# Kernel optimization log

Measured on AMD Instinct MI355X. Metric: run time of the kernel, lower is better.

## Reference

```python
import jax, jax.numpy as jnp
import numpy as np

B, N, S, T_STEPS = 8, 150, 22, 1000
E = 2 * N - 1  # 299
M = 32


def quat_mul(a, b):
    # Hamilton product, quats as (w, x, y, z)
    aw, ax, ay, az = a[..., 0], a[..., 1], a[..., 2], a[..., 3]
    bw, bx, by, bz = b[..., 0], b[..., 1], b[..., 2], b[..., 3]
    return jnp.stack([
        aw * bw - ax * bx - ay * by - az * bz,
        aw * bx + ax * bw + ay * bz - az * by,
        aw * by - ax * bz + ay * bw + az * bx,
        aw * bz + ax * by - ay * bx + az * bw,
    ], axis=-1)


def quat_conj(q):
    return q * jnp.array([1.0, -1.0, -1.0, -1.0], q.dtype)


def quat_rotate(q, v):
    # rotate vector v by unit quaternion q
    w, qv = q[..., :1], q[..., 1:]
    t = 2.0 * jnp.cross(qv, v)
    return v + w * t + jnp.cross(qv, t)


def egnn_layer(q, x, h, e, mask_f, Wm, bm, Wf, bf, Wq, bq):
    Bb, Nn = h.shape[0], h.shape[-2]
    eye = jnp.eye(Nn, dtype=h.dtype)
    mm = mask_f[:, :, None] * mask_f[:, None, :] * (1.0 - eye)  # [B,N,N]
    n_nodes = mask_f.sum(-1)  # [B]
    q_i = q[:, :, None, :]
    q_j = q[:, None, :, :]
    x_i = x[:, :, None, :]
    x_j = x[:, None, :, :]
    qj_inv = quat_conj(q_j)
    diff = x_i - x_j                              # [B,N,N,3]
    local_x = quat_rotate(qj_inv, diff)           # R_j^T (x_i - x_j)
    local_q = quat_mul(quat_mul(qj_inv, q_i), q_j)  # q_j^-1 q_i q_j
    d2 = jnp.sum(diff * diff, -1)                 # [B,N,N]
    dot = jnp.abs(jnp.sum(q_i * q_j, -1))         # [B,N,N]
    hi = jnp.broadcast_to(h[:, :, None, :], (Bb, Nn, Nn, h.shape[-1]))
    hj = jnp.broadcast_to(h[:, None, :, :], (Bb, Nn, Nn, h.shape[-1]))
    feat = jnp.concatenate([hi, hj, e, local_x, local_q, d2[..., None], dot[..., None]], -1)
    m = (feat @ Wm + bm) * mm[..., None]          # [B,N,N,M]
    o = jnp.concatenate([h, m.sum(-2)], -1) @ Wf + bf
    delta = (m @ Wq + bq) * mm[..., None]         # [B,N,N,6]
    upd_x = (quat_rotate(q_j, local_x + delta[..., 3:]) + x_j).sum(-2) \
        / (n_nodes[:, None, None] - 1.0)
    vec_q = jnp.concatenate([jnp.zeros_like(delta[..., :1]), delta[..., :3]], -1)
    s = (local_q + quat_mul(local_q, vec_q)).sum(-2)  # [B,N,4]
    local_upd_q = s / jnp.maximum(jnp.linalg.norm(s, axis=-1, keepdims=True), 1e-12)
    upd_q = quat_mul(quat_mul(q, local_upd_q), quat_conj(q))
    return upd_q, upd_x, o


def relposenc():
    r = jnp.arange(N)
    rel = N - 1 + (r[:, None] - r[None, :])
    return jax.nn.one_hot(rel, E, dtype=jnp.float32)  # [N,N,E]


def setup_inputs() -> dict:
    key = jax.random.key(0)
    ks = jax.random.split(key, 32)
    quats = jax.random.normal(ks[0], (B, N, 4), dtype=jnp.float32)
    quats = quats / jnp.linalg.norm(quats, axis=-1, keepdims=True)
    trans = jax.random.normal(ks[1], (B, N, 3), dtype=jnp.float32) * 10.0
    features = jax.random.uniform(ks[2], (B, N, S), dtype=jnp.float32)
    mask = jnp.ones((B, N), dtype=bool)
    inp = {"quats": quats, "trans": trans, "features": features, "mask": mask, "t": 250}
    # (message_in, feature_in, feature_out) per layer; H1=30, I=64
    dims = [(2 * 30 + E + 9, 30 + M, 64), (2 * 64 + E + 9, 64 + M, 64),
            (2 * 64 + E + 9, 64 + M, 64), (2 * 64 + E + 9, 64 + M, 1)]
    k = 3
    for i, (mi, fi, fo) in enumerate(dims, 1):
        inp[f"wm{i}"] = jax.random.normal(ks[k], (mi, M), dtype=jnp.float32) / np.float32(np.sqrt(mi)); k += 1
        inp[f"bm{i}"] = jnp.zeros((M,), jnp.float32)
        inp[f"wf{i}"] = jax.random.normal(ks[k], (fi, fo), dtype=jnp.float32) / np.float32(np.sqrt(fi)); k += 1
        inp[f"bf{i}"] = jnp.zeros((fo,), jnp.float32)
        inp[f"wq{i}"] = jax.random.normal(ks[k], (M, 6), dtype=jnp.float32) / np.float32(np.sqrt(M)); k += 1
        inp[f"bq{i}"] = jnp.zeros((6,), jnp.float32)
    return inp


def reference(quats, trans, features,
              wm1, bm1, wf1, bf1, wq1, bq1,
              wm2, bm2, wf2, bf2, wq2, bq2,
              wm3, bm3, wf3, bf3, wq3, bq3,
              wm4, bm4, wf4, bf4, wq4, bq4,
              mask, t):
    mask_f = mask.astype(quats.dtype)
    ft = jnp.full((B, N, 1), t / T_STEPS, dtype=quats.dtype)
    h = jnp.concatenate([quats, trans, features, ft], -1)  # [B,N,30]
    e = jnp.broadcast_to(relposenc()[None], (B, N, N, E))
    q, x = quats, trans
    q, x, i1 = egnn_layer(q, x, h, e, mask_f, wm1, bm1, wf1, bf1, wq1, bq1)
    q, x, i2 = egnn_layer(q, x, jax.nn.relu(i1), e, mask_f, wm2, bm2, wf2, bf2, wq2, bq2)
    q, x, i3 = egnn_layer(q, x, jax.nn.relu(i2), e, mask_f, wm3, bm3, wf3, bf3, wq3, bq3)
    q, x, _ = egnn_layer(q, x, jax.nn.relu(i3), e, mask_f, wm4, bm4, wf4, bf4, wq4, bq4)
    return jnp.concatenate([q, x], -1)  # tensor_7 of final frames [B,N,7]
```

## Files before the change

kernel.cpp:

```cpp
#include <hip/hip_runtime.h>
#include <math.h>

#define NB 8
#define NN 150
#define NE 299
#define NNODE (NB*NN)

struct Quat { float w, x, y, z; };

__device__ inline Quat qmul(Quat a, Quat b) {
    Quat r;
    r.w = a.w*b.w - a.x*b.x - a.y*b.y - a.z*b.z;
    r.x = a.w*b.x + a.x*b.w + a.y*b.z - a.z*b.y;
    r.y = a.w*b.y - a.x*b.z + a.y*b.w + a.z*b.x;
    r.z = a.w*b.z + a.x*b.y - a.y*b.x + a.z*b.w;
    return r;
}
__device__ inline Quat qconj(Quat a) { return Quat{a.w, -a.x, -a.y, -a.z}; }

__device__ inline float3 qrot(Quat q, float3 v) {
    float tx = 2.f*(q.y*v.z - q.z*v.y);
    float ty = 2.f*(q.z*v.x - q.x*v.z);
    float tz = 2.f*(q.x*v.y - q.y*v.x);
    float cx = q.y*tz - q.z*ty;
    float cy = q.z*tx - q.x*tz;
    float cz = q.x*ty - q.y*tx;
    float3 r;
    r.x = v.x + q.w*tx + cx;
    r.y = v.y + q.w*ty + cy;
    r.z = v.z + q.w*tz + cz;
    return r;
}

struct InitArgs {
    const float* quats; const float* trans; const float* feats; const int* tptr;
    const float* wm[4]; const float* wq[4];
    const float* bm1; const float* bq1;
    float* h; float* A; float* C0; float* Ad; float* Cd0;
    float* P; float* Ed; float* Gq;
};

__global__ __launch_bounds__(256) void init_kernel(InitArgs a)
{
    __shared__ float sh[8][30];
    __shared__ float sA[8][32];
    __shared__ float sC[8][32];
    __shared__ float sPS[256];
    const int tid = threadIdx.x;
    const int blk = blockIdx.x;

    if (blk < 150) {
        const int nodeBase = blk*8;
        for (int idx = tid; idx < 8*30; idx += 256) {
            const int nl = idx / 30;
            const int d  = idx - nl*30;
            const int n  = nodeBase + nl;
            float v;
            if      (d < 4)  v = a.quats[n*4 + d];
            else if (d < 7)  v = a.trans[n*3 + (d-4)];
            else if (d < 29) v = a.feats[n*22 + (d-7)];
            else             v = (float)a.tptr[0] * (1.0f/1000.0f);
            sh[nl][d] = v;
            a.h[n*64 + d] = v;
        }
        __syncthreads();
        {
            const int nl = tid >> 5;
            const int k  = tid & 31;
            const int n  = nodeBase + nl;
            float av = a.bm1[k], cv = 0.f;
#pragma unroll
            for (int d = 0; d < 30; ++d) {
                const float hv = sh[nl][d];
                av = fmaf(hv, a.wm[0][d*32 + k], av);
                cv = fmaf(hv, a.wm[0][(30+d)*32 + k], cv);
            }
            a.A[n*32 + k]  = av;
            a.C0[n*32 + k] = cv;
            sA[nl][k] = av;
            sC[nl][k] = cv;
        }
        __syncthreads();
        if (tid < 96) {
            const int half = (tid >= 48) ? 1 : 0;
            const int idx  = tid - half*48;
            const int nl = idx / 6;
            const int d  = idx - nl*6;
            const float* src = half ? sC[nl] : sA[nl];
            float acc = half ? 0.f : a.bq1[d];
#pragma unroll
            for (int k = 0; k < 32; ++k) acc = fmaf(src[k], a.wq[0][k*6 + d], acc);
            (half ? a.Cd0 : a.Ad)[(nodeBase+nl)*8 + d] = acc;
        }
    } else if (blk < 154) {
        const int l = blk - 150;
        const int HDl = (l == 0) ? 30 : 64;
        const float* E = a.wm[l] + 2*HDl*32;
        float* Pl = a.P + l*9600;
        const int g = tid >> 5, k = tid & 31;
        const int r0 = g*38;
        float part = 0.f;
        for (int r = r0; r < r0+38 && r < NE; ++r) part += E[r*32 + k];
        sPS[g*32 + k] = part;
        __syncthreads();
        float run = 0.f;
        for (int gg = 0; gg < g; ++gg) run += sPS[gg*32 + k];
        const int rw = (r0+38 < 300) ? r0+38 : 300;
        for (int r = r0; r < rw; ++r) {
            Pl[r*32 + k] = run;
            if (r < NE) run += E[r*32 + k];
        }
    } else if (blk < 158) {
        const int l = blk - 154;
        const int HDl = (l == 0) ? 30 : 64;
        const float* E  = a.wm[l] + 2*HDl*32;
        const float* Wq = a.wq[l];
        if (tid < 54) {
            const int t = tid/6, d = tid - t*6;
            float acc = 0.f;
#pragma unroll
            for (int k = 0; k < 32; ++k) acc = fmaf(E[(NE+t)*32 + k], Wq[k*6 + d], acc);
            a.Gq[l*64 + t*6 + d] = acc;
        }
    } else {
        const int bb = blk - 158;
        const int l = bb / 25;
        const int rbase = (bb % 25) * 12;
        const int HDl = (l == 0) ? 30 : 64;
        const float* E  = a.wm[l] + 2*HDl*32;
        const float* Wq = a.wq[l];
        if (tid < 72) {
            const int rr = tid/6, d = tid - rr*6;
            const int r = rbase + rr;
            if (r < NE) {
                float acc = 0.f;
#pragma unroll
                for (int k = 0; k < 32; ++k) acc = fmaf(E[r*32 + k], Wq[k*6 + d], acc);
                a.Ed[l*2400 + r*8 + d] = acc;
            }
        }
    }
}

struct PairArgs {
    const float* qcur; const float* xcur;
    const float* hbuf; const float* Abuf;
    const float* Cin;  const float* Adin; const float* Cdin;
    const float* Ed;   const float* Gq;   const float* P;
    const float* wm;   const float* wf;   const float* bf;
    const float* wmN;  const float* bmN;
    const float* wqN;  const float* bqN;
    float* hout; float* Aout; float* Adout;
    float* Cout; float* Cdout;
    float* qout; float* xout; float* dout;
};

template<int HD, bool COMPUTE_O, bool WRITE_OUT>
__global__ __launch_bounds__(192, 4) void pair_kernel(PairArgs a)
{
    constexpr int STR  = 196;
    constexpr int NROW = COMPUTE_O ? 32 : 7;
    constexpr int NV   = COMPUTE_O ? 16 : 7;
    __shared__ __align__(16) float sMat[NROW*STR];
    __shared__ float sWmG[COMPUTE_O ? 288 : 4];
    __shared__ float sPr[192];
    __shared__ float sTot[16];
    __shared__ float sCs[32];
    __shared__ float sHi[64], sO[64], sMs[32];
    __shared__ float sGq[54], sAd[6];
    __shared__ float sA2[32], sC2[32];

    const int tid   = threadIdx.x;
    const int nodeI = blockIdx.x;
    const int b     = nodeI / NN;
    const int i     = nodeI - b*NN;

    if (COMPUTE_O) {
        for (int idx = tid; idx < 288; idx += 192) sWmG[idx] = a.wm[(2*HD+NE)*32 + idx];
        for (int idx = tid; idx < HD;  idx += 192) sHi[idx]  = a.hbuf[nodeI*64 + idx];
    }
    if (tid < 54) sGq[tid] = a.Gq[tid];
    if (tid >= 64 && tid < 70) sAd[tid-64] = a.Adin[nodeI*8 + (tid-64)];
    __syncthreads();

    const Quat  qi = {a.qcur[nodeI*4+0], a.qcur[nodeI*4+1],
                      a.qcur[nodeI*4+2], a.qcur[nodeI*4+3]};
    const float3 xi = {a.xcur[nodeI*3+0], a.xcur[nodeI*3+1], a.xcur[nodeI*3+2]};

    float vals[NV];
#pragma unroll
    for (int v = 0; v < NV; ++v) vals[v] = 0.f;

    const int j = tid;
    Quat qj = {1.f,0.f,0.f,0.f};
    const float mm = (j == i) ? 0.f : 1.f;
    if (j < NN) {
        const int nodeJ = b*NN + j;
        qj = Quat{a.qcur[nodeJ*4+0], a.qcur[nodeJ*4+1],
                  a.qcur[nodeJ*4+2], a.qcur[nodeJ*4+3]};
        float3 xj = {a.xcur[nodeJ*3+0], a.xcur[nodeJ*3+1], a.xcur[nodeJ*3+2]};
        float3 diff = {xi.x - xj.x, xi.y - xj.y, xi.z - xj.z};
        Quat qjc = qconj(qj);
        float3 lx = qrot(qjc, diff);
        Quat lq = qmul(qmul(qjc, qi), qj);
        const float d2 = diff.x*diff.x + diff.y*diff.y + diff.z*diff.z;
        const float dt = fabsf(qi.w*qj.w + qi.x*qj.x + qi.y*qj.y + qi.z*qj.z);
        const float g[9] = {lx.x, lx.y, lx.z, lq.w, lq.x, lq.y, lq.z, d2, dt};

        const float4* cd4 = (const float4*)(a.Cdin + nodeJ*8);
        const float4* ed4 = (const float4*)(a.Ed + (NN-1 + i - j)*8);
        const float4 c0 = cd4[0], c1 = cd4[1];
        const float4 e0 = ed4[0], e1 = ed4[1];
        float delta[6];
        delta[0] = sAd[0] + c0.x + e0.x;
        delta[1] = sAd[1] + c0.y + e0.y;
        delta[2] = sAd[2] + c0.z + e0.z;
        delta[3] = sAd[3] + c0.w + e0.w;
        delta[4] = sAd[4] + c1.x + e1.x;
        delta[5] = sAd[5] + c1.y + e1.y;
#pragma unroll
        for (int t = 0; t < 9; ++t) {
            const float gv = g[t];
#pragma unroll
            for (int d = 0; d < 6; ++d)
                delta[d] = fmaf(gv, sGq[t*6 + d], delta[d]);
        }
#pragma unroll
        for (int d = 0; d < 6; ++d) delta[d] *= mm;

        constexpr int vo = COMPUTE_O ? 9 : 0;
        if (COMPUTE_O) {
#pragma unroll
            for (int t = 0; t < 9; ++t) vals[t] = g[t]*mm;
        }
        float3 dv = {delta[3], delta[4], delta[5]};
        float3 rd = qrot(qj, dv);
        vals[vo+0] = rd.x; vals[vo+1] = rd.y; vals[vo+2] = rd.z;
        Quat vq = {0.f, delta[0], delta[1], delta[2]};
        Quat sp = qmul(lq, vq);
        vals[vo+3] = lq.w + sp.w;
        vals[vo+4] = lq.x + sp.x;
        vals[vo+5] = lq.y + sp.y;
        vals[vo+6] = lq.z + sp.z;
    }

#pragma unroll
    for (int v = 0; v < NV; ++v) sMat[v*STR + tid] = vals[v];
    if (COMPUTE_O) {
        if (j < NN) {
            const float4* c4p = (const float4*)(a.Cin + (b*NN+j)*32);
#pragma unroll
            for (int q = 0; q < 4; ++q) {
                const float4 c = c4p[q];
                sMat[(16+4*q+0)*STR + tid] = c.x*mm;
                sMat[(16+4*q+1)*STR + tid] = c.y*mm;
                sMat[(16+4*q+2)*STR + tid] = c.z*mm;
                sMat[(16+4*q+3)*STR + tid] = c.w*mm;
            }
        } else {
#pragma unroll
            for (int r = 16; r < 32; ++r) sMat[r*STR + tid] = 0.f;
        }
    }
    __syncthreads();
    if (tid < 4*NROW) {
        const int ch = tid >> 2, q4 = tid & 3;
        const float4* row = (const float4*)(sMat + ch*STR + q4*48);
        float s0 = 0.f, s1 = 0.f, s2 = 0.f, s3 = 0.f;
#pragma unroll
        for (int it = 0; it < 12; ++it) {
            const float4 r = row[it];
            s0 += r.x; s1 += r.y; s2 += r.z; s3 += r.w;
        }
        sPr[tid] = (s0+s1) + (s2+s3);
    }
    __syncthreads();

    if (COMPUTE_O) {
        if (j < NN) {
            const float4* c4p = (const float4*)(a.Cin + (b*NN+j)*32);
#pragma unroll
            for (int q = 0; q < 4; ++q) {
                const float4 c = c4p[4+q];
                sMat[(4*q+0)*STR + tid] = c.x*mm;
                sMat[(4*q+1)*STR + tid] = c.y*mm;
                sMat[(4*q+2)*STR + tid] = c.z*mm;
                sMat[(4*q+3)*STR + tid] = c.w*mm;
            }
        } else {
#pragma unroll
            for (int r = 0; r < 16; ++r) sMat[r*STR + tid] = 0.f;
        }
        __syncthreads();
        if (tid < 64) {
            const int ch = tid >> 2, q4 = tid & 3;
            const float4* row = (const float4*)(sMat + ch*STR + q4*48);
            float s0 = 0.f, s1 = 0.f, s2 = 0.f, s3 = 0.f;
#pragma unroll
            for (int it = 0; it < 12; ++it) {
                const float4 r = row[it];
                s0 += r.x; s1 += r.y; s2 += r.z; s3 += r.w;
            }
            sPr[128 + tid] = (s0+s1) + (s2+s3);
        }
        __syncthreads();
    }

    if (COMPUTE_O) {
        if (tid < 16)
            sTot[tid] = (sPr[4*tid] + sPr[4*tid+1]) + (sPr[4*tid+2] + sPr[4*tid+3]);
        else if (tid < 32) {
            const int c = tid - 16, o4 = 64 + 4*c;
            sCs[c] = (sPr[o4] + sPr[o4+1]) + (sPr[o4+2] + sPr[o4+3]);
        } else if (tid < 48) {
            const int c = tid - 16, o4 = 128 + 4*(tid-32);
            sCs[c] = (sPr[o4] + sPr[o4+1]) + (sPr[o4+2] + sPr[o4+3]);
        }
    } else {
        if (tid < 7)
            sTot[tid] = (sPr[4*tid] + sPr[4*tid+1]) + (sPr[4*tid+2] + sPr[4*tid+3]);
    }
    __syncthreads();

    if (COMPUTE_O) {
        if (tid < 32) {
            const int k = tid;
            float ms = 149.f*a.Abuf[nodeI*32 + k] + sCs[k]
                     + a.P[(i+NN)*32 + k] - a.P[i*32 + k]
                     - a.wm[(2*HD + (NN-1))*32 + k];
#pragma unroll
            for (int t = 0; t < 9; ++t) ms = fmaf(sTot[t], sWmG[t*32 + k], ms);
            sMs[k] = ms;
        }
        __syncthreads();
        if (tid < 64) {
            float acc0 = a.bf[tid], acc1 = 0.f;
#pragma unroll 8
            for (int d = 0; d < HD; d += 2) {
                acc0 = fmaf(sHi[d],   a.wf[d*64 + tid],     acc0);
                acc1 = fmaf(sHi[d+1], a.wf[(d+1)*64 + tid], acc1);
            }
#pragma unroll 8
            for (int k = 0; k < 32; k += 2) {
                acc0 = fmaf(sMs[k],   a.wf[(HD+k)*64 + tid],   acc0);
                acc1 = fmaf(sMs[k+1], a.wf[(HD+k+1)*64 + tid], acc1);
            }
            sO[tid] = acc0 + acc1;
        }
    }

    if (tid == 0) {
        constexpr int XO = COMPUTE_O ? 9 : 0;
        const float inv = 1.0f / (float)(NN - 1);
        const float ux0 = ((float)NN * xi.x + sTot[XO+0]) * inv;
        const float ux1 = ((float)NN * xi.y + sTot[XO+1]) * inv;
        const float ux2 = ((float)NN * xi.z + sTot[XO+2]) * inv;
        Quat s = {sTot[XO+3], sTot[XO+4], sTot[XO+5], sTot[XO+6]};
        const float nrm = sqrtf(s.w*s.w + s.x*s.x + s.y*s.y + s.z*s.z);
        const float invn = 1.0f / fmaxf(nrm, 1e-12f);
        Quat u = {s.w*invn, s.x*invn, s.y*invn, s.z*invn};
        Quat uq = qmul(qmul(qi, u), qconj(qi));
        if (WRITE_OUT) {
            float* op = a.dout + nodeI*7;
            op[0] = uq.w; op[1] = uq.x; op[2] = uq.y; op[3] = uq.z;
            op[4] = ux0;  op[5] = ux1;  op[6] = ux2;
        } else {
            a.qout[nodeI*4+0] = uq.w; a.qout[nodeI*4+1] = uq.x;
            a.qout[nodeI*4+2] = uq.y; a.qout[nodeI*4+3] = uq.z;
            a.xout[nodeI*3+0] = ux0;  a.xout[nodeI*3+1] = ux1;
            a.xout[nodeI*3+2] = ux2;
        }
    }

    if (COMPUTE_O) {
        __syncthreads();
        if (tid < 64) {
            const float hn = fmaxf(sO[tid], 0.f);
            sHi[tid] = hn;
            a.hout[nodeI*64 + tid] = hn;
        }
        __syncthreads();
        if (tid < 64) {
            const int k   = tid & 31;
            const int off = (tid >= 32) ? 64 : 0;
            float acc = (tid < 32) ? a.bmN[k] : 0.f;
#pragma unroll
            for (int d = 0; d < 64; ++d) acc = fmaf(sHi[d], a.wmN[(off+d)*32 + k], acc);
            if (tid < 32) { a.Aout[nodeI*32 + k] = acc; sA2[k] = acc; }
            else          { a.Cout[nodeI*32 + k] = acc; sC2[k] = acc; }
        }
        __syncthreads();
        if (tid < 12) {
            const int half = (tid >= 6) ? 1 : 0;
            const int d = tid - half*6;
            const float* src = half ? sC2 : sA2;
            float acc = half ? 0.f : a.bqN[d];
#pragma unroll
            for (int k = 0; k < 32; ++k) acc = fmaf(src[k], a.wqN[k*6 + d], acc);
            (half ? a.Cdout : a.Adout)[nodeI*8 + d] = acc;
        }
    }
}


extern "C" void kernel_launch(void* const* d_in, const int* in_sizes, int n_in,
                              void* d_out, int out_size, void* d_ws, size_t ws_size,
                              hipStream_t stream) {
    const float* wm[4] = {(const float*)d_in[5],  (const float*)d_in[11],
                          (const float*)d_in[17], (const float*)d_in[23]};
    const float* bm[4] = {(const float*)d_in[6],  (const float*)d_in[12],
                          (const float*)d_in[18], (const float*)d_in[24]};
    const float* wf[4] = {(const float*)d_in[7],  (const float*)d_in[13],
                          (const float*)d_in[19], (const float*)d_in[25]};
    const float* bf[4] = {(const float*)d_in[8],  (const float*)d_in[14],
                          (const float*)d_in[20], (const float*)d_in[26]};
    const float* wq[4] = {(const float*)d_in[9],  (const float*)d_in[15],
                          (const float*)d_in[21], (const float*)d_in[27]};
    const float* bq[4] = {(const float*)d_in[10], (const float*)d_in[16],
                          (const float*)d_in[22], (const float*)d_in[28]};

    float* ws = (float*)d_ws;
    float* h   = ws;
    float* A   = h   + NNODE*64;
    float* C0  = A   + NNODE*32;
    float* C1  = C0  + NNODE*32;
    float* Ad  = C1  + NNODE*32;
    float* Cd0 = Ad  + NNODE*8;
    float* Cd1 = Cd0 + NNODE*8;
    float* qA  = Cd1 + NNODE*8;
    float* xA  = qA  + NNODE*4;
    float* qB  = xA  + NNODE*3;
    float* xB  = qB  + NNODE*4;
    float* Pp  = xB  + NNODE*3;
    float* Edp = Pp  + 4*9600;
    float* Gqp = Edp + 4*2400;

    InitArgs ia;
    ia.quats = (const float*)d_in[0];
    ia.trans = (const float*)d_in[1];
    ia.feats = (const float*)d_in[2];
    ia.tptr  = (const int*)d_in[4];
    for (int l = 0; l < 4; ++l) { ia.wm[l] = wm[l]; ia.wq[l] = wq[l]; }
    ia.bm1 = bm[0]; ia.bq1 = bq[0];
    ia.h = h; ia.A = A; ia.C0 = C0; ia.Ad = Ad; ia.Cd0 = Cd0;
    ia.P = Pp; ia.Ed = Edp; ia.Gq = Gqp;
    init_kernel<<<dim3(258), dim3(256), 0, stream>>>(ia);

    PairArgs p;
    p.hout = h; p.Aout = A; p.Adout = Ad;
    p.dout = (float*)d_out;

    p.qcur = (const float*)d_in[0]; p.xcur = (const float*)d_in[1];
    p.hbuf = h; p.Abuf = A; p.Cin = C0; p.Adin = Ad; p.Cdin = Cd0;
    p.Ed = Edp + 0*2400; p.Gq = Gqp + 0*64; p.P = Pp + 0*9600;
    p.wm = wm[0]; p.wf = wf[0]; p.bf = bf[0];
    p.wmN = wm[1]; p.bmN = bm[1]; p.wqN = wq[1]; p.bqN = bq[1];
    p.Cout = C1; p.Cdout = Cd1;
    p.qout = qA; p.xout = xA;
    pair_kernel<30, true, false><<<dim3(NNODE), dim3(192), 0, stream>>>(p);

    p.qcur = qA; p.xcur = xA;
    p.Cin = C1; p.Cdin = Cd1;
    p.Ed = Edp + 1*2400; p.Gq = Gqp + 1*64; p.P = Pp + 1*9600;
    p.wm = wm[1]; p.wf = wf[1]; p.bf = bf[1];
    p.wmN = wm[2]; p.bmN = bm[2]; p.wqN = wq[2]; p.bqN = bq[2];
    p.Cout = C0; p.Cdout = Cd0;
    p.qout = qB; p.xout = xB;
    pair_kernel<64, true, false><<<dim3(NNODE), dim3(192), 0, stream>>>(p);

    p.qcur = qB; p.xcur = xB;
    p.Cin = C0; p.Cdin = Cd0;
    p.Ed = Edp + 2*2400; p.Gq = Gqp + 2*64; p.P = Pp + 2*9600;
    p.wm = wm[2]; p.wf = wf[2]; p.bf = bf[2];
    p.wmN = wm[3]; p.bmN = bm[3]; p.wqN = wq[3]; p.bqN = bq[3];
    p.Cout = C1; p.Cdout = Cd1;
    p.qout = qA; p.xout = xA;
    pair_kernel<64, true, false><<<dim3(NNODE), dim3(192), 0, stream>>>(p);

    p.qcur = qA; p.xcur = xA;
    p.Cin = C1; p.Cdin = Cd1;
    p.Ed = Edp + 3*2400; p.Gq = Gqp + 3*64; p.P = Pp + 3*9600;
    p.wm = wm[3]; p.wf = wf[3]; p.bf = bf[3];
    p.wmN = wm[3]; p.bmN = bm[3]; p.wqN = wq[3]; p.bqN = bq[3];
    p.Cout = C0; p.Cdout = Cd0;
    p.qout = nullptr; p.xout = nullptr;
    pair_kernel<64, false, true><<<dim3(NNODE), dim3(192), 0, stream>>>(p);
}
```

Before: 167.5 us.

## Replace per-node C-row reduction with precomputed per-batch column sums

Each pair block no longer reloads and reduces all 150 neighbour C rows (32 channels) through shared memory. Instead it uses a per-batch sum of C, computed in init for layer 1 and accumulated with atomicAdd in the previous layer's tail, then subtracts its own row. This removes two reduction passes, shrinks shared memory and raises launch bounds occupancy from 4 to 5. It also drops writes of h/A/C that the next layer does not need, and moves the q/x output to a thread that runs in parallel with the tail. Atomic accumulation changes summation order and makes the Csum buffers depend on zero-initialisation in init.

```diff
diff --git a/kernel.cpp b/kernel.cpp
--- a/kernel.cpp
+++ b/kernel.cpp
@@ -37,7 +37,7 @@
     const float* wm[4]; const float* wq[4];
     const float* bm1; const float* bq1;
     float* h; float* A; float* C0; float* Ad; float* Cd0;
-    float* P; float* Ed; float* Gq;
+    float* P; float* Ed; float* Gq; float* Csum;
 };
 
 __global__ __launch_bounds__(256) void init_kernel(InitArgs a)
@@ -122,7 +122,7 @@
             for (int k = 0; k < 32; ++k) acc = fmaf(E[(NE+t)*32 + k], Wq[k*6 + d], acc);
             a.Gq[l*64 + t*6 + d] = acc;
         }
-    } else {
+    } else if (blk < 258) {
         const int bb = blk - 158;
         const int l = bb / 25;
         const int rbase = (bb % 25) * 12;
@@ -139,33 +139,48 @@
                 a.Ed[l*2400 + r*8 + d] = acc;
             }
         }
+    } else {
+        if (tid < 240) {
+            const int bb = tid/30, d = tid - bb*30;
+            float acc = 0.f;
+            if (d < 4)       { for (int jj=0;jj<NN;++jj) acc += a.quats[(bb*NN+jj)*4 + d]; }
+            else if (d < 7)  { for (int jj=0;jj<NN;++jj) acc += a.trans[(bb*NN+jj)*3 + (d-4)]; }
+            else if (d < 29) { for (int jj=0;jj<NN;++jj) acc += a.feats[(bb*NN+jj)*22 + (d-7)]; }
+            else             { acc = (float)NN * ((float)a.tptr[0] * (1.0f/1000.0f)); }
+            sh[bb][d] = acc;
+        }
+        a.Csum[256 + tid] = 0.f;
+        a.Csum[512 + tid] = 0.f;
+        a.Csum[768 + tid] = 0.f;
+        __syncthreads();
+        const int bb = tid >> 5, k = tid & 31;
+        float acc = 0.f;
+#pragma unroll
+        for (int d = 0; d < 30; ++d) acc = fmaf(sh[bb][d], a.wm[0][(30+d)*32 + k], acc);
+        a.Csum[bb*32 + k] = acc;
     }
 }
 
 struct PairArgs {
     const float* qcur; const float* xcur;
-    const float* hbuf; const float* Abuf;
-    const float* Cin;  const float* Adin; const float* Cdin;
-    const float* Ed;   const float* Gq;   const float* P;
-    const float* wm;   const float* wf;   const float* bf;
-    const float* wmN;  const float* bmN;
-    const float* wqN;  const float* bqN;
-    float* hout; float* Aout; float* Adout;
-    float* Cout; float* Cdout;
+    const float* hbuf; const float* Abuf; const float* Cin;
+    const float* Adin; const float* Cdin;
+    const float* Ed; const float* Gq; const float* P; const float* Csum;
+    const float* wm; const float* wf; const float* bf;
+    const float* wmN; const float* bmN; const float* wqN; const float* bqN;
+    float* hout; float* Aout; float* Adout; float* Cout; float* Cdout;
+    float* CsumN;
     float* qout; float* xout; float* dout;
 };
 
-template<int HD, bool COMPUTE_O, bool WRITE_OUT>
-__global__ __launch_bounds__(192, 4) void pair_kernel(PairArgs a)
+template<int HD, bool COMPUTE_O, bool WRITE_OUT, bool TAIL_FULL>
+__global__ __launch_bounds__(192, 5) void pair_kernel(PairArgs a)
 {
-    constexpr int STR  = 196;
-    constexpr int NROW = COMPUTE_O ? 32 : 7;
-    constexpr int NV   = COMPUTE_O ? 16 : 7;
-    __shared__ __align__(16) float sMat[NROW*STR];
-    __shared__ float sWmG[COMPUTE_O ? 288 : 4];
-    __shared__ float sPr[192];
+    constexpr int STR = 196;
+    constexpr int NV  = COMPUTE_O ? 16 : 7;
+    __shared__ __align__(16) float sMat[NV*STR];
+    __shared__ float sPr[64];
     __shared__ float sTot[16];
-    __shared__ float sCs[32];
     __shared__ float sHi[64], sO[64], sMs[32];
     __shared__ float sGq[54], sAd[6];
     __shared__ float sA2[32], sC2[32];
@@ -174,38 +189,35 @@
     const int nodeI = blockIdx.x;
     const int b     = nodeI / NN;
     const int i     = nodeI - b*NN;
-
-    if (COMPUTE_O) {
-        for (int idx = tid; idx < 288; idx += 192) sWmG[idx] = a.wm[(2*HD+NE)*32 + idx];
-        for (int idx = tid; idx < HD;  idx += 192) sHi[idx]  = a.hbuf[nodeI*64 + idx];
-    }
+    const int j     = tid;
+
+    if (COMPUTE_O) { if (tid < HD) sHi[tid] = a.hbuf[nodeI*64 + tid]; }
     if (tid < 54) sGq[tid] = a.Gq[tid];
     if (tid >= 64 && tid < 70) sAd[tid-64] = a.Adin[nodeI*8 + (tid-64)];
     __syncthreads();
 
-    const Quat  qi = {a.qcur[nodeI*4+0], a.qcur[nodeI*4+1],
-                      a.qcur[nodeI*4+2], a.qcur[nodeI*4+3]};
+    const float4 qi4 = ((const float4*)a.qcur)[nodeI];
+    const Quat  qi = {qi4.x, qi4.y, qi4.z, qi4.w};
     const float3 xi = {a.xcur[nodeI*3+0], a.xcur[nodeI*3+1], a.xcur[nodeI*3+2]};
 
     float vals[NV];
 #pragma unroll
     for (int v = 0; v < NV; ++v) vals[v] = 0.f;
 
-    const int j = tid;
-    Quat qj = {1.f,0.f,0.f,0.f};
-    const float mm = (j == i) ? 0.f : 1.f;
     if (j < NN) {
         const int nodeJ = b*NN + j;
-        qj = Quat{a.qcur[nodeJ*4+0], a.qcur[nodeJ*4+1],
-                  a.qcur[nodeJ*4+2], a.qcur[nodeJ*4+3]};
+        const float4 q4 = ((const float4*)a.qcur)[nodeJ];
+        Quat qj = {q4.x, q4.y, q4.z, q4.w};
         float3 xj = {a.xcur[nodeJ*3+0], a.xcur[nodeJ*3+1], a.xcur[nodeJ*3+2]};
+        const float mm = (j == i) ? 0.f : 1.f;
+
         float3 diff = {xi.x - xj.x, xi.y - xj.y, xi.z - xj.z};
         Quat qjc = qconj(qj);
         float3 lx = qrot(qjc, diff);
         Quat lq = qmul(qmul(qjc, qi), qj);
-        const float d2 = diff.x*diff.x + diff.y*diff.y + diff.z*diff.z;
+        const float d2v = diff.x*diff.x + diff.y*diff.y + diff.z*diff.z;
         const float dt = fabsf(qi.w*qj.w + qi.x*qj.x + qi.y*qj.y + qi.z*qj.z);
-        const float g[9] = {lx.x, lx.y, lx.z, lq.w, lq.x, lq.y, lq.z, d2, dt};
+        const float g[9] = {lx.x, lx.y, lx.z, lq.w, lq.x, lq.y, lq.z, d2v, dt};
 
         const float4* cd4 = (const float4*)(a.Cdin + nodeJ*8);
         const float4* ed4 = (const float4*)(a.Ed + (NN-1 + i - j)*8);
@@ -222,11 +234,11 @@
         for (int t = 0; t < 9; ++t) {
             const float gv = g[t];
 #pragma unroll
-            for (int d = 0; d < 6; ++d)
-                delta[d] = fmaf(gv, sGq[t*6 + d], delta[d]);
-        }
-#pragma unroll
-        for (int d = 0; d < 6; ++d) delta[d] *= mm;
+            for (int d2 = 0; d2 < 6; ++d2)
+                delta[d2] = fmaf(gv, sGq[t*6 + d2], delta[d2]);
+        }
+#pragma unroll
+        for (int d2 = 0; d2 < 6; ++d2) delta[d2] *= mm;
 
         constexpr int vo = COMPUTE_O ? 9 : 0;
         if (COMPUTE_O) {
@@ -246,26 +258,10 @@
 
 #pragma unroll
     for (int v = 0; v < NV; ++v) sMat[v*STR + tid] = vals[v];
-    if (COMPUTE_O) {
-        if (j < NN) {
-            const float4* c4p = (const float4*)(a.Cin + (b*NN+j)*32);
-#pragma unroll
-            for (int q = 0; q < 4; ++q) {
-                const float4 c = c4p[q];
-                sMat[(16+4*q+0)*STR + tid] = c.x*mm;
-                sMat[(16+4*q+1)*STR + tid] = c.y*mm;
-                sMat[(16+4*q+2)*STR + tid] = c.z*mm;
-                sMat[(16+4*q+3)*STR + tid] = c.w*mm;
-            }
-        } else {
-#pragma unroll
-            for (int r = 16; r < 32; ++r) sMat[r*STR + tid] = 0.f;
-        }
-    }
     __syncthreads();
-    if (tid < 4*NROW) {
-        const int ch = tid >> 2, q4 = tid & 3;
-        const float4* row = (const float4*)(sMat + ch*STR + q4*48);
+    if (tid < 4*NV) {
+        const int ch = tid >> 2, q4i = tid & 3;
+        const float4* row = (const float4*)(sMat + ch*STR + q4i*48);
         float s0 = 0.f, s1 = 0.f, s2 = 0.f, s3 = 0.f;
 #pragma unroll
         for (int it = 0; it < 12; ++it) {
@@ -275,70 +271,44 @@
         sPr[tid] = (s0+s1) + (s2+s3);
     }
     __syncthreads();
-
-    if (COMPUTE_O) {
-        if (j < NN) {
-            const float4* c4p = (const float4*)(a.Cin + (b*NN+j)*32);
-#pragma unroll
-            for (int q = 0; q < 4; ++q) {
-                const float4 c = c4p[4+q];
-                sMat[(4*q+0)*STR + tid] = c.x*mm;
-                sMat[(4*q+1)*STR + tid] = c.y*mm;
-                sMat[(4*q+2)*STR + tid] = c.z*mm;
-                sMat[(4*q+3)*STR + tid] = c.w*mm;
-            }
-        } else {
-#pragma unroll
-            for (int r = 0; r < 16; ++r) sMat[r*STR + tid] = 0.f;
-        }
-        __syncthreads();
-        if (tid < 64) {
-            const int ch = tid >> 2, q4 = tid & 3;
-            const float4* row = (const float4*)(sMat + ch*STR + q4*48);
-            float s0 = 0.f, s1 = 0.f, s2 = 0.f, s3 = 0.f;
-#pragma unroll
-            for (int it = 0; it < 12; ++it) {
-                const float4 r = row[it];
-                s0 += r.x; s1 += r.y; s2 += r.z; s3 += r.w;
-            }
-            sPr[128 + tid] = (s0+s1) + (s2+s3);
-        }
-        __syncthreads();
-    }
-
-    if (COMPUTE_O) {
-        if (tid < 16)
-            sTot[tid] = (sPr[4*tid] + sPr[4*tid+1]) + (sPr[4*tid+2] + sPr[4*tid+3]);
-        else if (tid < 32) {
-            const int c = tid - 16, o4 = 64 + 4*c;
-            sCs[c] = (sPr[o4] + sPr[o4+1]) + (sPr[o4+2] + sPr[o4+3]);
-        } else if (tid < 48) {
-            const int c = tid - 16, o4 = 128 + 4*(tid-32);
-            sCs[c] = (sPr[o4] + sPr[o4+1]) + (sPr[o4+2] + sPr[o4+3]);
-        }
-    } else {
-        if (tid < 7)
-            sTot[tid] = (sPr[4*tid] + sPr[4*tid+1]) + (sPr[4*tid+2] + sPr[4*tid+3]);
-    }
+    if (tid < NV)
+        sTot[tid] = (sPr[4*tid] + sPr[4*tid+1]) + (sPr[4*tid+2] + sPr[4*tid+3]);
     __syncthreads();
 
     if (COMPUTE_O) {
         if (tid < 32) {
             const int k = tid;
-            float ms = 149.f*a.Abuf[nodeI*32 + k] + sCs[k]
+            float ms = 149.f*a.Abuf[nodeI*32 + k]
+                     + a.Csum[b*32 + k] - a.Cin[nodeI*32 + k]
                      + a.P[(i+NN)*32 + k] - a.P[i*32 + k]
                      - a.wm[(2*HD + (NN-1))*32 + k];
 #pragma unroll
-            for (int t = 0; t < 9; ++t) ms = fmaf(sTot[t], sWmG[t*32 + k], ms);
+            for (int t = 0; t < 9; ++t)
+                ms = fmaf(sTot[t], a.wm[(2*HD + NE + t)*32 + k], ms);
             sMs[k] = ms;
+        }
+        if (tid == 64) {
+            const float inv = 1.0f / (float)(NN - 1);
+            const float ux0 = ((float)NN * xi.x + sTot[9])  * inv;
+            const float ux1 = ((float)NN * xi.y + sTot[10]) * inv;
+            const float ux2 = ((float)NN * xi.z + sTot[11]) * inv;
+            Quat s = {sTot[12], sTot[13], sTot[14], sTot[15]};
+            const float nrm = sqrtf(s.w*s.w + s.x*s.x + s.y*s.y + s.z*s.z);
+            const float invn = 1.0f / fmaxf(nrm, 1e-12f);
+            Quat u = {s.w*invn, s.x*invn, s.y*invn, s.z*invn};
+            Quat uq = qmul(qmul(qi, u), qconj(qi));
+            a.qout[nodeI*4+0] = uq.w; a.qout[nodeI*4+1] = uq.x;
+            a.qout[nodeI*4+2] = uq.y; a.qout[nodeI*4+3] = uq.z;
+            a.xout[nodeI*3+0] = ux0;  a.xout[nodeI*3+1] = ux1;
+            a.xout[nodeI*3+2] = ux2;
         }
         __syncthreads();
         if (tid < 64) {
             float acc0 = a.bf[tid], acc1 = 0.f;
 #pragma unroll 8
-            for (int d = 0; d < HD; d += 2) {
-                acc0 = fmaf(sHi[d],   a.wf[d*64 + tid],     acc0);
-                acc1 = fmaf(sHi[d+1], a.wf[(d+1)*64 + tid], acc1);
+            for (int d2 = 0; d2 < HD; d2 += 2) {
+                acc0 = fmaf(sHi[d2],   a.wf[d2*64 + tid],     acc0);
+                acc1 = fmaf(sHi[d2+1], a.wf[(d2+1)*64 + tid], acc1);
             }
 #pragma unroll 8
             for (int k = 0; k < 32; k += 2) {
@@ -347,37 +317,11 @@
             }
             sO[tid] = acc0 + acc1;
         }
-    }
-
-    if (tid == 0) {
-        constexpr int XO = COMPUTE_O ? 9 : 0;
-        const float inv = 1.0f / (float)(NN - 1);
-        const float ux0 = ((float)NN * xi.x + sTot[XO+0]) * inv;
-        const float ux1 = ((float)NN * xi.y + sTot[XO+1]) * inv;
-        const float ux2 = ((float)NN * xi.z + sTot[XO+2]) * inv;
-        Quat s = {sTot[XO+3], sTot[XO+4], sTot[XO+5], sTot[XO+6]};
-        const float nrm = sqrtf(s.w*s.w + s.x*s.x + s.y*s.y + s.z*s.z);
-        const float invn = 1.0f / fmaxf(nrm, 1e-12f);
-        Quat u = {s.w*invn, s.x*invn, s.y*invn, s.z*invn};
-        Quat uq = qmul(qmul(qi, u), qconj(qi));
-        if (WRITE_OUT) {
-            float* op = a.dout + nodeI*7;
-            op[0] = uq.w; op[1] = uq.x; op[2] = uq.y; op[3] = uq.z;
-            op[4] = ux0;  op[5] = ux1;  op[6] = ux2;
-        } else {
-            a.qout[nodeI*4+0] = uq.w; a.qout[nodeI*4+1] = uq.x;
-            a.qout[nodeI*4+2] = uq.y; a.qout[nodeI*4+3] = uq.z;
-            a.xout[nodeI*3+0] = ux0;  a.xout[nodeI*3+1] = ux1;
-            a.xout[nodeI*3+2] = ux2;
-        }
-    }
-
-    if (COMPUTE_O) {
         __syncthreads();
         if (tid < 64) {
             const float hn = fmaxf(sO[tid], 0.f);
             sHi[tid] = hn;
-            a.hout[nodeI*64 + tid] = hn;
+            if (TAIL_FULL) a.hout[nodeI*64 + tid] = hn;
         }
         __syncthreads();
         if (tid < 64) {
@@ -385,19 +329,50 @@
             const int off = (tid >= 32) ? 64 : 0;
             float acc = (tid < 32) ? a.bmN[k] : 0.f;
 #pragma unroll
-            for (int d = 0; d < 64; ++d) acc = fmaf(sHi[d], a.wmN[(off+d)*32 + k], acc);
-            if (tid < 32) { a.Aout[nodeI*32 + k] = acc; sA2[k] = acc; }
-            else          { a.Cout[nodeI*32 + k] = acc; sC2[k] = acc; }
+            for (int d2 = 0; d2 < 64; ++d2)
+                acc = fmaf(sHi[d2], a.wmN[(off+d2)*32 + k], acc);
+            if (tid < 32) {
+                sA2[k] = acc;
+                if (TAIL_FULL) a.Aout[nodeI*32 + k] = acc;
+            } else {
+                sC2[k] = acc;
+                if (TAIL_FULL) {
+                    a.Cout[nodeI*32 + k] = acc;
+                    atomicAdd(&a.CsumN[b*32 + k], acc);
+                }
+            }
         }
         __syncthreads();
         if (tid < 12) {
             const int half = (tid >= 6) ? 1 : 0;
-            const int d = tid - half*6;
+            const int d2 = tid - half*6;
             const float* src = half ? sC2 : sA2;
-            float acc = half ? 0.f : a.bqN[d];
-#pragma unroll
-            for (int k = 0; k < 32; ++k) acc = fmaf(src[k], a.wqN[k*6 + d], acc);
-            (half ? a.Cdout : a.Adout)[nodeI*8 + d] = acc;
+            float acc = half ? 0.f : a.bqN[d2];
+#pragma unroll
+            for (int k = 0; k < 32; ++k) acc = fmaf(src[k], a.wqN[k*6 + d2], acc);
+            (half ? a.Cdout : a.Adout)[nodeI*8 + d2] = acc;
+        }
+    } else {
+        if (tid == 0) {
+            const float inv = 1.0f / (float)(NN - 1);
+            const float ux0 = ((float)NN * xi.x + sTot[0]) * inv;
+            const float ux1 = ((float)NN * xi.y + sTot[1]) * inv;
+            const float ux2 = ((float)NN * xi.z + sTot[2]) * inv;
+            Quat s = {sTot[3], sTot[4], sTot[5], sTot[6]};
+            const float nrm = sqrtf(s.w*s.w + s.x*s.x + s.y*s.y + s.z*s.z);
+            const float invn = 1.0f / fmaxf(nrm, 1e-12f);
+            Quat u = {s.w*invn, s.x*invn, s.y*invn, s.z*invn};
+            Quat uq = qmul(qmul(qi, u), qconj(qi));
+            if (WRITE_OUT) {
+                float* op = a.dout + nodeI*7;
+                op[0] = uq.w; op[1] = uq.x; op[2] = uq.y; op[3] = uq.z;
+                op[4] = ux0;  op[5] = ux1;  op[6] = ux2;
+            } else {
+                a.qout[nodeI*4+0] = uq.w; a.qout[nodeI*4+1] = uq.x;
+                a.qout[nodeI*4+2] = uq.y; a.qout[nodeI*4+3] = uq.z;
+                a.xout[nodeI*3+0] = ux0;  a.xout[nodeI*3+1] = ux1;
+                a.xout[nodeI*3+2] = ux2;
+            }
         }
     }
 }
@@ -406,6 +381,8 @@
 extern "C" void kernel_launch(void* const* d_in, const int* in_sizes, int n_in,
                               void* d_out, int out_size, void* d_ws, size_t ws_size,
                               hipStream_t stream) {
+    const float* quats = (const float*)d_in[0];
+    const float* trans = (const float*)d_in[1];
     const float* wm[4] = {(const float*)d_in[5],  (const float*)d_in[11],
                           (const float*)d_in[17], (const float*)d_in[23]};
     const float* bm[4] = {(const float*)d_in[6],  (const float*)d_in[12],
@@ -422,67 +399,68 @@
     float* ws = (float*)d_ws;
     float* h   = ws;
     float* A   = h   + NNODE*64;
-    float* C0  = A   + NNODE*32;
-    float* C1  = C0  + NNODE*32;
-    float* Ad  = C1  + NNODE*32;
-    float* Cd0 = Ad  + NNODE*8;
-    float* Cd1 = Cd0 + NNODE*8;
-    float* qA  = Cd1 + NNODE*8;
+    float* CA  = A   + NNODE*32;
+    float* CB  = CA  + NNODE*32;
+    float* Ad  = CB  + NNODE*32;
+    float* CdA = Ad  + NNODE*8;
+    float* CdB = CdA + NNODE*8;
+    float* qA  = CdB + NNODE*8;
     float* xA  = qA  + NNODE*4;
     float* qB  = xA  + NNODE*3;
     float* xB  = qB  + NNODE*4;
     float* Pp  = xB  + NNODE*3;
     float* Edp = Pp  + 4*9600;
     float* Gqp = Edp + 4*2400;
+    float* Cs  = Gqp + 256;
 
     InitArgs ia;
-    ia.quats = (const float*)d_in[0];
-    ia.trans = (const float*)d_in[1];
+    ia.quats = quats; ia.trans = trans;
     ia.feats = (const float*)d_in[2];
     ia.tptr  = (const int*)d_in[4];
     for (int l = 0; l < 4; ++l) { ia.wm[l] = wm[l]; ia.wq[l] = wq[l]; }
     ia.bm1 = bm[0]; ia.bq1 = bq[0];
-    ia.h = h; ia.A = A; ia.C0 = C0; ia.Ad = Ad; ia.Cd0 = Cd0;
-    ia.P = Pp; ia.Ed = Edp; ia.Gq = Gqp;
-    init_kernel<<<dim3(258), dim3(256), 0, stream>>>(ia);
+    ia.h = h; ia.A = A; ia.C0 = CA; ia.Ad = Ad; ia.Cd0 = CdA;
+    ia.P = Pp; ia.Ed = Edp; ia.Gq = Gqp; ia.Csum = Cs;
+    init_kernel<<<dim3(259), dim3(256), 0, stream>>>(ia);
 
     PairArgs p;
-    p.hout = h; p.Aout = A; p.Adout = Ad;
     p.dout = (float*)d_out;
 
-    p.qcur = (const float*)d_in[0]; p.xcur = (const float*)d_in[1];
-    p.hbuf = h; p.Abuf = A; p.Cin = C0; p.Adin = Ad; p.Cdin = Cd0;
-    p.Ed = Edp + 0*2400; p.Gq = Gqp + 0*64; p.P = Pp + 0*9600;
+    p.qcur = quats; p.xcur = trans;
+    p.hbuf = h; p.Abuf = A; p.Cin = CA; p.Adin = Ad; p.Cdin = CdA;
+    p.Ed = Edp + 0*2400; p.Gq = Gqp + 0*64; p.P = Pp + 0*9600; p.Csum = Cs + 0*256;
     p.wm = wm[0]; p.wf = wf[0]; p.bf = bf[0];
     p.wmN = wm[1]; p.bmN = bm[1]; p.wqN = wq[1]; p.bqN = bq[1];
-    p.Cout = C1; p.Cdout = Cd1;
+    p.hout = h; p.Aout = A; p.Adout = Ad; p.Cout = CB; p.Cdout = CdB;
+    p.CsumN = Cs + 1*256;
     p.qout = qA; p.xout = xA;
-    pair_kernel<30, true, false><<<dim3(NNODE), dim3(192), 0, stream>>>(p);
+    pair_kernel<30, true, false, true><<<dim3(NNODE), dim3(192), 0, stream>>>(p);
 
     p.qcur = qA; p.xcur = xA;
-    p.Cin = C1; p.Cdin = Cd1;
-    p.Ed = Edp + 1*2400; p.Gq = Gqp + 1*64; p.P = Pp + 1*9600;
+    p.Cin = CB; p.Cdin = CdB;
+    p.Ed = Edp + 1*2400; p.Gq = Gqp + 1*64; p.P = Pp + 1*9600; p.Csum = Cs + 1*256;
     p.wm = wm[1]; p.wf = wf[1]; p.bf = bf[1];
     p.wmN = wm[2]; p.bmN = bm[2]; p.wqN = wq[2]; p.bqN = bq[2];
-    p.Cout = C0; p.Cdout = Cd0;
+    p.Cout = CA; p.Cdout = CdA;
+    p.CsumN = Cs + 2*256;
     p.qout = qB; p.xout = xB;
-    pair_kernel<64, true, false><<<dim3(NNODE), dim3(192), 0, stream>>>(p);
+    pair_kernel<64, true, false, true><<<dim3(NNODE), dim3(192), 0, stream>>>(p);
 
     p.qcur = qB; p.xcur = xB;
-    p.Cin = C0; p.Cdin = Cd0;
-    p.Ed = Edp + 2*2400; p.Gq = Gqp + 2*64; p.P = Pp + 2*9600;
+    p.Cin = CA; p.Cdin = CdA;
+    p.Ed = Edp + 2*2400; p.Gq = Gqp + 2*64; p.P = Pp + 2*9600; p.Csum = Cs + 2*256;
     p.wm = wm[2]; p.wf = wf[2]; p.bf = bf[2];
     p.wmN = wm[3]; p.bmN = bm[3]; p.wqN = wq[3]; p.bqN = bq[3];
-    p.Cout = C1; p.Cdout = Cd1;
+    p.Cout = CB; p.Cdout = CdB;
+    p.CsumN = Cs + 3*256;
     p.qout = qA; p.xout = xA;
-    pair_kernel<64, true, false><<<dim3(NNODE), dim3(192), 0, stream>>>(p);
+    pair_kernel<64, true, false, false><<<dim3(NNODE), dim3(192), 0, stream>>>(p);
 
     p.qcur = qA; p.xcur = xA;
-    p.Cin = C1; p.Cdin = Cd1;
-    p.Ed = Edp + 3*2400; p.Gq = Gqp + 3*64; p.P = Pp + 3*9600;
+    p.Cin = CB; p.Cdin = CdB; p.Adin = Ad;
+    p.Ed = Edp + 3*2400; p.Gq = Gqp + 3*64; p.P = Pp + 3*9600; p.Csum = Cs + 3*256;
     p.wm = wm[3]; p.wf = wf[3]; p.bf = bf[3];
     p.wmN = wm[3]; p.bmN = bm[3]; p.wqN = wq[3]; p.bqN = bq[3];
-    p.Cout = C0; p.Cdout = Cd0;
     p.qout = nullptr; p.xout = nullptr;
-    pair_kernel<64, false, true><<<dim3(NNODE), dim3(192), 0, stream>>>(p);
+    pair_kernel<64, false, true, false><<<dim3(NNODE), dim3(192), 0, stream>>>(p);
 }
```

Result: no change. 165.3 us, median of 2 (-1.3%).
